# Performance work log

Measured on AMD Instinct MI355X. Metric: run time of the kernel, lower is better.

The kernel has to match this reference:

```python
import jax, jax.numpy as jnp
import numpy as np

# Module config (matches init_kwargs)
DIM = 256
NUM_HEADS = 8
AREA = 4
B, C, H, W = 8, DIM, 64, 64
HEAD_DIM = DIM // NUM_HEADS

# Each Conv in the source is Conv2d(bias=False) + BatchNorm2d + Identity (activation=False).
# In eval mode BN is a per-channel affine, so we represent each Conv as (weight, scale, bias).

def setup_inputs() -> dict:
    key = jax.random.key(0)
    ks = jax.random.split(key, 13)
    def w(k, shape, s=0.05):
        return jax.random.normal(k, shape, jnp.float32) * s
    def bn_scale(k, n):
        return 1.0 + 0.02 * jax.random.normal(k, (n,), jnp.float32)
    x = jax.random.normal(ks[0], (B, C, H, W), jnp.float32)
    return {
        "x": x,
        "w_qk": w(ks[1], (2 * C, C)),        # 1x1 conv: [out,in]
        "s_qk": bn_scale(ks[2], 2 * C),
        "b_qk": w(ks[3], (2 * C,), 0.01),
        "w_v": w(ks[4], (C, C)),
        "s_v": bn_scale(ks[5], C),
        "b_v": w(ks[6], (C,), 0.01),
        "w_pe": w(ks[7], (C, 1, 5, 5)),       # depthwise 5x5, groups=C
        "s_pe": bn_scale(ks[8], C),
        "b_pe": w(ks[9], (C,), 0.01),
        "w_proj": w(ks[10], (C, C)),
        "s_proj": bn_scale(ks[11], C),
        "b_proj": w(ks[12], (C,), 0.01),
    }


def _affine(y, s, b):
    # per-channel BN-eval affine on NCHW
    return y * s[None, :, None, None] + b[None, :, None, None]


def _conv1x1(x, w, s, b):
    return _affine(jnp.einsum('bchw,oc->bohw', x, w), s, b)


def reference(x, w_qk, s_qk, b_qk, w_v, s_v, b_v, w_pe, s_pe, b_pe, w_proj, s_proj, b_proj):
    N = H * W
    Na = N // AREA
    Ba = B * AREA

    qk = _conv1x1(x, w_qk, s_qk, b_qk)                    # [B, 2C, H, W]
    v4 = _conv1x1(x, w_v, s_v, b_v)                       # [B, C, H, W]
    pp = _affine(
        jax.lax.conv_general_dilated(
            v4, w_pe, (1, 1), 'SAME', feature_group_count=C,
            dimension_numbers=('NCHW', 'OIHW', 'NCHW')),
        s_pe, b_pe)                                        # [B, C, H, W]

    # flatten(2).transpose(1,2) then area split along N
    qk = qk.reshape(B, 2 * C, N).transpose(0, 2, 1).reshape(Ba, Na, 2 * C)
    v = v4.reshape(B, C, N).transpose(0, 2, 1).reshape(Ba, Na, C)

    q = qk[..., :C].reshape(Ba, Na, NUM_HEADS, HEAD_DIM)
    k = qk[..., C:].reshape(Ba, Na, NUM_HEADS, HEAD_DIM)
    vh = v.reshape(Ba, Na, NUM_HEADS, HEAD_DIM)

    scale = jnp.asarray(HEAD_DIM, jnp.float32) ** -0.5
    attn = jnp.einsum('bqhd,bkhd->bhqk', q, k) * scale     # [Ba, h, Na, Na]
    attn = jax.nn.softmax(attn, axis=-1)                   # max-stable softmax over keys
    o = jnp.einsum('bhqk,bkhd->bqhd', attn, vh)            # [Ba, Na, h, d]
    o = o.reshape(Ba, Na, C).reshape(B, N, C)
    o = o.reshape(B, H, W, C).transpose(0, 3, 1, 2)        # [B, C, H, W]

    return _conv1x1(o + pp, w_proj, s_proj, b_proj)
```

## Files before the change

### kernel.cpp

```cpp
#include <hip/hip_runtime.h>
#include <math.h>


#define NN 4096
#define NA 1024

typedef unsigned short us;
typedef __attribute__((ext_vector_type(4))) unsigned short us4;
typedef __attribute__((ext_vector_type(8))) unsigned short us8;
typedef __attribute__((ext_vector_type(8))) short bf16x8;
typedef __attribute__((ext_vector_type(4))) float f32x4;

#define QS (0.17677669529663687f * 1.4426950408889634f)

__device__ __forceinline__ us f2b(float f) {
    unsigned u = __builtin_bit_cast(unsigned, f);
    u += 0x7fffu + ((u >> 16) & 1u);
    return (us)(u >> 16);
}
__device__ __forceinline__ float b2f(us h) {
    unsigned u = ((unsigned)h) << 16;
    return __builtin_bit_cast(float, u);
}
__device__ __forceinline__ unsigned pack2(float lo, float hi) {
    return (unsigned)f2b(lo) | ((unsigned)f2b(hi) << 16);
}
__device__ __forceinline__ unsigned cvtpk_bf16(float lo, float hi) {
    unsigned r;
    asm("v_cvt_pk_bf16_f32 %0, %1, %2" : "=v"(r) : "v"(lo), "v"(hi));
    return r;
}

__global__ __launch_bounds__(256) void prep_kernel(
    const float* __restrict__ w_qk, const float* __restrict__ s_qk, const float* __restrict__ b_qk,
    const float* __restrict__ w_v,  const float* __restrict__ s_v,
    const float* __restrict__ w_proj, const float* __restrict__ s_proj,
    us* __restrict__ wqkh, us* __restrict__ wvh, us* __restrict__ wprojh,
    float* __restrict__ bqkp)
{
    int idx = blockIdx.x * 256 + threadIdx.x;
    if (idx < 131072) {
        int o = idx >> 8;
        float sc = s_qk[o] * (o < 256 ? QS : 1.0f);
        wqkh[idx] = f2b(w_qk[idx] * sc);
    } else if (idx < 196608) {
        int j = idx - 131072; int o = j >> 8;
        wvh[j] = f2b(w_v[j] * s_v[o]);
    } else {
        int j = idx - 196608; int o = j >> 8;
        wprojh[j] = f2b(w_proj[j] * s_proj[o]);
    }
    if (idx < 512) bqkp[idx] = b_qk[idx] * (idx < 256 ? QS : 1.0f);
}

__global__ __launch_bounds__(256) void qkv_kernel(
    const float* __restrict__ x,
    const us* __restrict__ wqkh, const float* __restrict__ bqkp,
    const us* __restrict__ wvh,  const float* __restrict__ b_v,
    us* __restrict__ qt, us* __restrict__ vbuf)
{
    const int n0 = blockIdx.x * 64;
    const int b  = blockIdx.y;
    const int tid = threadIdx.x;
    const int w = tid >> 6, lane = tid & 63, c = lane & 15, g = lane >> 4;

    __shared__ __align__(16) us Xs[64][264];

    const float* Xb = x + (size_t)b * 256 * NN;
    #pragma unroll
    for (int i = 0; i < 16; i++) {
        int t = tid + i * 256;
        int cp = t >> 5, pp = t & 31;
        const float* r0 = Xb + (size_t)(2 * cp) * NN + n0 + 2 * pp;
        float2 a0 = *(const float2*)r0;
        float2 a1 = *(const float2*)(r0 + NN);
        *(unsigned*)&Xs[2 * pp][2 * cp]     = pack2(a0.x, a1.x);
        *(unsigned*)&Xs[2 * pp + 1][2 * cp] = pack2(a0.y, a1.y);
    }
    __syncthreads();

    for (int grp = 0; grp < 3; grp++) {
        f32x4 acc[4][4] = {};
        for (int kc = 0; kc < 256; kc += 32) {
            bf16x8 Xf[4];
            #pragma unroll
            for (int j = 0; j < 4; j++)
                Xf[j] = *(const bf16x8*)&Xs[j * 16 + c][kc + g * 8];
            #pragma unroll
            for (int cgi = 0; cgi < 4; cgi++) {
                int ch = (grp < 2 ? (grp * 4 + cgi) * 64 : cgi * 64) + w * 16 + c;
                const us* Wp = (grp < 2 ? wqkh : wvh) + (size_t)ch * 256 + kc + g * 8;
                bf16x8 Wf = *(const bf16x8*)Wp;
                if (grp < 2) {
                    #pragma unroll
                    for (int j = 0; j < 4; j++)
                        acc[cgi][j] = __builtin_amdgcn_mfma_f32_16x16x32_bf16(Xf[j], Wf, acc[cgi][j], 0, 0, 0);
                } else {
                    #pragma unroll
                    for (int j = 0; j < 4; j++)
                        acc[cgi][j] = __builtin_amdgcn_mfma_f32_16x16x32_bf16(Wf, Xf[j], acc[cgi][j], 0, 0, 0);
                }
            }
        }
        if (grp < 2) {
            #pragma unroll
            for (int cgi = 0; cgi < 4; cgi++) {
                int ch = (grp * 4 + cgi) * 64 + w * 16 + c;
                float bb = bqkp[ch];
                #pragma unroll
                for (int j = 0; j < 4; j++)
                    #pragma unroll
                    for (int r = 0; r < 4; r++)
                        qt[((size_t)b * 4096 + n0 + j * 16 + g * 4 + r) * 512 + ch] =
                            f2b(acc[cgi][j][r] + bb);
            }
        } else {
            #pragma unroll
            for (int cgi = 0; cgi < 4; cgi++)
                #pragma unroll
                for (int r = 0; r < 4; r++) {
                    int ch = cgi * 64 + w * 16 + g * 4 + r;
                    float bb = b_v[ch];
                    #pragma unroll
                    for (int j = 0; j < 4; j++)
                        vbuf[((size_t)b * 256 + ch) * NN + n0 + j * 16 + c] =
                            f2b(acc[cgi][j][r] + bb);
                }
        }
    }
}

__global__ __launch_bounds__(256) void pe_conv_kernel(
    const us* __restrict__ vbuf,
    const float* __restrict__ w_pe, const float* __restrict__ s_pe, const float* __restrict__ b_pe,
    float* __restrict__ opp)
{
    const int c = blockIdx.x, b = blockIdx.y;
    const int tid = threadIdx.x;
    const us* vp = vbuf + ((size_t)b * 256 + c) * NN;
    __shared__ float plane[4096];
    __shared__ float wloc[25];
    #pragma unroll
    for (int i = 0; i < 4; i++) {
        int idx = tid + i * 256;
        us4 v = *(const us4*)&vp[idx * 4];
        float4 f;
        f.x = b2f(v[0]); f.y = b2f(v[1]); f.z = b2f(v[2]); f.w = b2f(v[3]);
        *(float4*)&plane[idx * 4] = f;
    }
    if (tid < 25) wloc[tid] = w_pe[c * 25 + tid];
    __syncthreads();

    const float s = s_pe[c], bb = b_pe[c];
    float* op = opp + ((size_t)b * 256 + c) * NN;
    for (int i = 0; i < 16; i++) {
        int pix = tid + i * 256;
        int ph = pix >> 6, pw = pix & 63;
        float acc = 0.f;
        #pragma unroll
        for (int dy = -2; dy <= 2; dy++) {
            int hy = ph + dy;
            if (hy < 0 || hy > 63) continue;
            #pragma unroll
            for (int dx = -2; dx <= 2; dx++) {
                int wx = pw + dx;
                if (wx < 0 || wx > 63) continue;
                acc += plane[hy * 64 + wx] * wloc[(dy + 2) * 5 + (dx + 2)];
            }
        }
        op[pix] = acc * s + bb;
    }
}

__global__ __launch_bounds__(256) void attn_kernel(
    const us* __restrict__ qt, const us* __restrict__ vbuf, float* __restrict__ opp)
{
    const int qtb = blockIdx.x;
    const int h   = blockIdx.y;
    const int ba  = blockIdx.z;
    const int b = ba >> 2, a = ba & 3;
    const int tid = threadIdx.x;
    const int w = tid >> 6, lane = tid & 63, c = lane & 15, g = lane >> 4;
    const int q0 = qtb * 64;

    __shared__ __align__(16) us Qt[64][40];
    __shared__ __align__(16) us Kt[2][64][40];
    __shared__ __align__(16) us Vs[2][2048];
    __shared__ __align__(16) us Ps[64][72];

    const int krow = tid >> 2, kseg = tid & 3;
    const int vrow = tid >> 3, vseg = tid & 7;
    const int vbyte = vrow * 128 + ((vseg ^ (vrow & 7)) << 4);

    const us* Kg = qt + ((size_t)b * 4096 + a * NA) * 512 + 256 + h * 32;
    const us* Vg = vbuf + ((size_t)b * 256 + h * 32) * NN + a * NA;

    {
        int row = tid >> 2, seg = tid & 3;
        *(us8*)&Qt[row][seg * 8] =
            *(const us8*)&qt[((size_t)b * 4096 + a * NA + q0 + row) * 512 + h * 32 + seg * 8];
    }
    {
        us8 kreg = *(const us8*)(Kg + (size_t)krow * 512 + kseg * 8);
        us8 vreg = *(const us8*)(Vg + (size_t)vrow * NN + vseg * 8);
        *(us8*)&Kt[0][krow][kseg * 8] = kreg;
        *(us8*)((char*)Vs[0] + vbyte) = vreg;
    }
    __syncthreads();

    const bf16x8 Qfrag = *(const bf16x8*)&Qt[w * 16 + c][g * 8];
    const bf16x8 ones = {0x3F80, 0x3F80, 0x3F80, 0x3F80, 0x3F80, 0x3F80, 0x3F80, 0x3F80};
    const f32x4 z = {0.f, 0.f, 0.f, 0.f};
    const int qr = w * 16 + c;

    f32x4 O0 = z, O1 = z, Osum = z;
    int cur = 0;

    for (int kt = 0; kt < 16; kt++) {
        us8 kreg, vreg;
        if (kt < 15) {
            const int kv1 = (kt + 1) * 64;
            kreg = *(const us8*)(Kg + ((size_t)(kv1 + krow)) * 512 + kseg * 8);
            vreg = *(const us8*)(Vg + (size_t)vrow * NN + kv1 + vseg * 8);
        }

        f32x4 sA[4];
        #pragma unroll
        for (int j = 0; j < 4; j++) {
            bf16x8 Kf = *(const bf16x8*)&Kt[cur][j * 16 + c][g * 8];
            sA[j] = __builtin_amdgcn_mfma_f32_16x16x32_bf16(Kf, Qfrag, z, 0, 0, 0);
        }

        #pragma unroll
        for (int j = 0; j < 4; j++) {
            uint2 pr;
            pr.x = cvtpk_bf16(exp2f(sA[j][0]), exp2f(sA[j][1]));
            pr.y = cvtpk_bf16(exp2f(sA[j][2]), exp2f(sA[j][3]));
            *(uint2*)&Ps[qr][j * 16 + g * 4] = pr;
        }

        asm volatile("s_waitcnt lgkmcnt(0)" ::: "memory");
        __builtin_amdgcn_sched_barrier(0);

        #pragma unroll
        for (int ks = 0; ks < 2; ks++) {
            bf16x8 Ap = *(const bf16x8*)&Ps[qr][ks * 32 + g * 8];
            int so = (((ks * 4 + g) ^ (c & 7)) << 4);
            bf16x8 Bv0 = *(const bf16x8*)((char*)Vs[cur] + c * 128 + so);
            bf16x8 Bv1 = *(const bf16x8*)((char*)Vs[cur] + (16 + c) * 128 + so);
            O0   = __builtin_amdgcn_mfma_f32_16x16x32_bf16(Ap, Bv0, O0, 0, 0, 0);
            O1   = __builtin_amdgcn_mfma_f32_16x16x32_bf16(Ap, Bv1, O1, 0, 0, 0);
            Osum = __builtin_amdgcn_mfma_f32_16x16x32_bf16(Ap, ones, Osum, 0, 0, 0);
        }

        if (kt < 15) {
            *(us8*)&Kt[cur ^ 1][krow][kseg * 8] = kreg;
            *(us8*)((char*)Vs[cur ^ 1] + vbyte) = vreg;
        }
        __syncthreads();
        cur ^= 1;
    }

    float linv[4];
    #pragma unroll
    for (int r = 0; r < 4; r++) linv[r] = 1.0f / Osum[r];

    float* Ob = opp + ((size_t)(b * 256 + h * 32)) * NN + a * NA + q0 + w * 16 + g * 4;
    {
        float4 o = *(float4*)(Ob + (size_t)c * NN);
        o.x += O0[0] * linv[0]; o.y += O0[1] * linv[1];
        o.z += O0[2] * linv[2]; o.w += O0[3] * linv[3];
        *(float4*)(Ob + (size_t)c * NN) = o;
        float4 o2 = *(float4*)(Ob + (size_t)(16 + c) * NN);
        o2.x += O1[0] * linv[0]; o2.y += O1[1] * linv[1];
        o2.z += O1[2] * linv[2]; o2.w += O1[3] * linv[3];
        *(float4*)(Ob + (size_t)(16 + c) * NN) = o2;
    }
}

__global__ __launch_bounds__(256) void proj_kernel(
    const float* __restrict__ opp,
    const us* __restrict__ wprojh, const float* __restrict__ b_proj,
    float* __restrict__ out)
{
    const int n0 = blockIdx.x * 64;
    const int b  = blockIdx.y;
    const int tid = threadIdx.x;
    const int w = tid >> 6, lane = tid & 63, c = lane & 15, g = lane >> 4;

    __shared__ __align__(16) us Xs[64][264];

    const float* Xb = opp + (size_t)b * 256 * NN;
    #pragma unroll
    for (int i = 0; i < 16; i++) {
        int t = tid + i * 256;
        int cp = t >> 5, pp = t & 31;
        const float* r0 = Xb + (size_t)(2 * cp) * NN + n0 + 2 * pp;
        float2 a0 = *(const float2*)r0;
        float2 a1 = *(const float2*)(r0 + NN);
        *(unsigned*)&Xs[2 * pp][2 * cp]     = pack2(a0.x, a1.x);
        *(unsigned*)&Xs[2 * pp + 1][2 * cp] = pack2(a0.y, a1.y);
    }
    __syncthreads();

    f32x4 acc[4][4] = {};
    for (int kc = 0; kc < 256; kc += 32) {
        bf16x8 Xf[4];
        #pragma unroll
        for (int j = 0; j < 4; j++)
            Xf[j] = *(const bf16x8*)&Xs[j * 16 + c][kc + g * 8];
        #pragma unroll
        for (int cgi = 0; cgi < 4; cgi++) {
            int ch = cgi * 64 + w * 16 + c;
            bf16x8 Wf = *(const bf16x8*)(wprojh + (size_t)ch * 256 + kc + g * 8);
            #pragma unroll
            for (int j = 0; j < 4; j++)
                acc[cgi][j] = __builtin_amdgcn_mfma_f32_16x16x32_bf16(Wf, Xf[j], acc[cgi][j], 0, 0, 0);
        }
    }

    #pragma unroll
    for (int cgi = 0; cgi < 4; cgi++)
        #pragma unroll
        for (int r = 0; r < 4; r++) {
            int ch = cgi * 64 + w * 16 + g * 4 + r;
            float bb = b_proj[ch];
            #pragma unroll
            for (int j = 0; j < 4; j++)
                out[((size_t)b * 256 + ch) * NN + n0 + j * 16 + c] = acc[cgi][j][r] + bb;
        }
}

extern "C" void kernel_launch(void* const* d_in, const int* in_sizes, int n_in,
                              void* d_out, int out_size, void* d_ws, size_t ws_size,
                              hipStream_t stream) {
    const float* x      = (const float*)d_in[0];
    const float* w_qk   = (const float*)d_in[1];
    const float* s_qk   = (const float*)d_in[2];
    const float* b_qk   = (const float*)d_in[3];
    const float* w_v    = (const float*)d_in[4];
    const float* s_v    = (const float*)d_in[5];
    const float* b_v    = (const float*)d_in[6];
    const float* w_pe   = (const float*)d_in[7];
    const float* s_pe   = (const float*)d_in[8];
    const float* b_pe   = (const float*)d_in[9];
    const float* w_proj = (const float*)d_in[10];
    const float* s_proj = (const float*)d_in[11];
    const float* b_proj = (const float*)d_in[12];
    float* out = (float*)d_out;

    char* p = (char*)d_ws;
    us* qtb     = (us*)p;                  p += (size_t)8 * 4096 * 512 * 2;
    us* vbuf    = (us*)p;                  p += (size_t)8 * 256 * 4096 * 2;
    float* opp  = (float*)p;               p += (size_t)8 * 256 * 4096 * 4;
    us* wqkh    = (us*)p;                  p += (size_t)512 * 256 * 2;
    us* wvh     = (us*)p;                  p += (size_t)256 * 256 * 2;
    us* wprojh  = (us*)p;                  p += (size_t)256 * 256 * 2;
    float* bqkp = (float*)p;

    prep_kernel<<<1024, 256, 0, stream>>>(w_qk, s_qk, b_qk, w_v, s_v,
                                          w_proj, s_proj, wqkh, wvh, wprojh, bqkp);
    qkv_kernel<<<dim3(64, 8), 256, 0, stream>>>(x, wqkh, bqkp, wvh, b_v, qtb, vbuf);
    pe_conv_kernel<<<dim3(256, 8), 256, 0, stream>>>(vbuf, w_pe, s_pe, b_pe, opp);
    attn_kernel<<<dim3(16, 8, 32), 256, 0, stream>>>(qtb, vbuf, opp);
    proj_kernel<<<dim3(64, 8), 256, 0, stream>>>(opp, wprojh, b_proj, out);
}
```

Baseline: 181.9 us.

## Process two query tiles per attention block and use raw v_exp_f32

```diff
diff --git a/kernel.cpp b/kernel.cpp
--- a/kernel.cpp
+++ b/kernel.cpp
@@ -28,6 +28,11 @@
 __device__ __forceinline__ unsigned cvtpk_bf16(float lo, float hi) {
     unsigned r;
     asm("v_cvt_pk_bf16_f32 %0, %1, %2" : "=v"(r) : "v"(lo), "v"(hi));
+    return r;
+}
+__device__ __forceinline__ float fexp2(float x) {
+    float r;
+    asm("v_exp_f32 %0, %1" : "=v"(r) : "v"(x));
     return r;
 }
 
@@ -181,12 +186,12 @@
     const int b = ba >> 2, a = ba & 3;
     const int tid = threadIdx.x;
     const int w = tid >> 6, lane = tid & 63, c = lane & 15, g = lane >> 4;
-    const int q0 = qtb * 64;
-
-    __shared__ __align__(16) us Qt[64][40];
+    const int q0 = qtb * 128;
+
+    __shared__ __align__(16) us Qt[128][40];
     __shared__ __align__(16) us Kt[2][64][40];
     __shared__ __align__(16) us Vs[2][2048];
-    __shared__ __align__(16) us Ps[64][72];
+    __shared__ __align__(16) us Ps[128][72];
 
     const int krow = tid >> 2, kseg = tid & 3;
     const int vrow = tid >> 3, vseg = tid & 7;
@@ -195,8 +200,10 @@
     const us* Kg = qt + ((size_t)b * 4096 + a * NA) * 512 + 256 + h * 32;
     const us* Vg = vbuf + ((size_t)b * 256 + h * 32) * NN + a * NA;
 
-    {
-        int row = tid >> 2, seg = tid & 3;
+    #pragma unroll
+    for (int i = 0; i < 2; i++) {
+        int t = tid + i * 256;
+        int row = t >> 2, seg = t & 3;
         *(us8*)&Qt[row][seg * 8] =
             *(const us8*)&qt[((size_t)b * 4096 + a * NA + q0 + row) * 512 + h * 32 + seg * 8];
     }
@@ -208,12 +215,14 @@
     }
     __syncthreads();
 
-    const bf16x8 Qfrag = *(const bf16x8*)&Qt[w * 16 + c][g * 8];
+    const bf16x8 Qf0 = *(const bf16x8*)&Qt[w * 16 + c][g * 8];
+    const bf16x8 Qf1 = *(const bf16x8*)&Qt[64 + w * 16 + c][g * 8];
     const bf16x8 ones = {0x3F80, 0x3F80, 0x3F80, 0x3F80, 0x3F80, 0x3F80, 0x3F80, 0x3F80};
     const f32x4 z = {0.f, 0.f, 0.f, 0.f};
-    const int qr = w * 16 + c;
-
-    f32x4 O0 = z, O1 = z, Osum = z;
+    const int qr0 = w * 16 + c, qr1 = 64 + w * 16 + c;
+
+    f32x4 O0a = z, O1a = z, Osa = z;
+    f32x4 O0b = z, O1b = z, Osb = z;
     int cur = 0;
 
     for (int kt = 0; kt < 16; kt++) {
@@ -224,19 +233,24 @@
             vreg = *(const us8*)(Vg + (size_t)vrow * NN + kv1 + vseg * 8);
         }
 
-        f32x4 sA[4];
+        f32x4 sA[4], sB[4];
         #pragma unroll
         for (int j = 0; j < 4; j++) {
             bf16x8 Kf = *(const bf16x8*)&Kt[cur][j * 16 + c][g * 8];
-            sA[j] = __builtin_amdgcn_mfma_f32_16x16x32_bf16(Kf, Qfrag, z, 0, 0, 0);
+            sA[j] = __builtin_amdgcn_mfma_f32_16x16x32_bf16(Kf, Qf0, z, 0, 0, 0);
+            sB[j] = __builtin_amdgcn_mfma_f32_16x16x32_bf16(Kf, Qf1, z, 0, 0, 0);
         }
 
         #pragma unroll
         for (int j = 0; j < 4; j++) {
             uint2 pr;
-            pr.x = cvtpk_bf16(exp2f(sA[j][0]), exp2f(sA[j][1]));
-            pr.y = cvtpk_bf16(exp2f(sA[j][2]), exp2f(sA[j][3]));
-            *(uint2*)&Ps[qr][j * 16 + g * 4] = pr;
+            pr.x = cvtpk_bf16(fexp2(sA[j][0]), fexp2(sA[j][1]));
+            pr.y = cvtpk_bf16(fexp2(sA[j][2]), fexp2(sA[j][3]));
+            *(uint2*)&Ps[qr0][j * 16 + g * 4] = pr;
+            uint2 qr_;
+            qr_.x = cvtpk_bf16(fexp2(sB[j][0]), fexp2(sB[j][1]));
+            qr_.y = cvtpk_bf16(fexp2(sB[j][2]), fexp2(sB[j][3]));
+            *(uint2*)&Ps[qr1][j * 16 + g * 4] = qr_;
         }
 
         asm volatile("s_waitcnt lgkmcnt(0)" ::: "memory");
@@ -244,13 +258,17 @@
 
         #pragma unroll
         for (int ks = 0; ks < 2; ks++) {
-            bf16x8 Ap = *(const bf16x8*)&Ps[qr][ks * 32 + g * 8];
             int so = (((ks * 4 + g) ^ (c & 7)) << 4);
             bf16x8 Bv0 = *(const bf16x8*)((char*)Vs[cur] + c * 128 + so);
             bf16x8 Bv1 = *(const bf16x8*)((char*)Vs[cur] + (16 + c) * 128 + so);
-            O0   = __builtin_amdgcn_mfma_f32_16x16x32_bf16(Ap, Bv0, O0, 0, 0, 0);
-            O1   = __builtin_amdgcn_mfma_f32_16x16x32_bf16(Ap, Bv1, O1, 0, 0, 0);
-            Osum = __builtin_amdgcn_mfma_f32_16x16x32_bf16(Ap, ones, Osum, 0, 0, 0);
+            bf16x8 Ap0 = *(const bf16x8*)&Ps[qr0][ks * 32 + g * 8];
+            bf16x8 Ap1 = *(const bf16x8*)&Ps[qr1][ks * 32 + g * 8];
+            O0a = __builtin_amdgcn_mfma_f32_16x16x32_bf16(Ap0, Bv0, O0a, 0, 0, 0);
+            O1a = __builtin_amdgcn_mfma_f32_16x16x32_bf16(Ap0, Bv1, O1a, 0, 0, 0);
+            Osa = __builtin_amdgcn_mfma_f32_16x16x32_bf16(Ap0, ones, Osa, 0, 0, 0);
+            O0b = __builtin_amdgcn_mfma_f32_16x16x32_bf16(Ap1, Bv0, O0b, 0, 0, 0);
+            O1b = __builtin_amdgcn_mfma_f32_16x16x32_bf16(Ap1, Bv1, O1b, 0, 0, 0);
+            Osb = __builtin_amdgcn_mfma_f32_16x16x32_bf16(Ap1, ones, Osb, 0, 0, 0);
         }
 
         if (kt < 15) {
@@ -261,20 +279,30 @@
         cur ^= 1;
     }
 
-    float linv[4];
-    #pragma unroll
-    for (int r = 0; r < 4; r++) linv[r] = 1.0f / Osum[r];
+    float linva[4], linvb[4];
+    #pragma unroll
+    for (int r = 0; r < 4; r++) { linva[r] = 1.0f / Osa[r]; linvb[r] = 1.0f / Osb[r]; }
 
     float* Ob = opp + ((size_t)(b * 256 + h * 32)) * NN + a * NA + q0 + w * 16 + g * 4;
     {
         float4 o = *(float4*)(Ob + (size_t)c * NN);
-        o.x += O0[0] * linv[0]; o.y += O0[1] * linv[1];
-        o.z += O0[2] * linv[2]; o.w += O0[3] * linv[3];
+        o.x += O0a[0] * linva[0]; o.y += O0a[1] * linva[1];
+        o.z += O0a[2] * linva[2]; o.w += O0a[3] * linva[3];
         *(float4*)(Ob + (size_t)c * NN) = o;
         float4 o2 = *(float4*)(Ob + (size_t)(16 + c) * NN);
-        o2.x += O1[0] * linv[0]; o2.y += O1[1] * linv[1];
-        o2.z += O1[2] * linv[2]; o2.w += O1[3] * linv[3];
+        o2.x += O1a[0] * linva[0]; o2.y += O1a[1] * linva[1];
+        o2.z += O1a[2] * linva[2]; o2.w += O1a[3] * linva[3];
         *(float4*)(Ob + (size_t)(16 + c) * NN) = o2;
+
+        float* Ob2 = Ob + 64;
+        float4 o3 = *(float4*)(Ob2 + (size_t)c * NN);
+        o3.x += O0b[0] * linvb[0]; o3.y += O0b[1] * linvb[1];
+        o3.z += O0b[2] * linvb[2]; o3.w += O0b[3] * linvb[3];
+        *(float4*)(Ob2 + (size_t)c * NN) = o3;
+        float4 o4 = *(float4*)(Ob2 + (size_t)(16 + c) * NN);
+        o4.x += O1b[0] * linvb[0]; o4.y += O1b[1] * linvb[1];
+        o4.z += O1b[2] * linvb[2]; o4.w += O1b[3] * linvb[3];
+        *(float4*)(Ob2 + (size_t)(16 + c) * NN) = o4;
     }
 }
 
@@ -362,6 +390,6 @@
                                           w_proj, s_proj, wqkh, wvh, wprojh, bqkp);
     qkv_kernel<<<dim3(64, 8), 256, 0, stream>>>(x, wqkh, bqkp, wvh, b_v, qtb, vbuf);
     pe_conv_kernel<<<dim3(256, 8), 256, 0, stream>>>(vbuf, w_pe, s_pe, b_pe, opp);
-    attn_kernel<<<dim3(16, 8, 32), 256, 0, stream>>>(qtb, vbuf, opp);
+    attn_kernel<<<dim3(8, 8, 32), 256, 0, stream>>>(qtb, vbuf, opp);
     proj_kernel<<<dim3(64, 8), 256, 0, stream>>>(opp, wprojh, b_proj, out);
 }
```

Result: faster. 159.7 us (-12.2%).
